# Kernel tuning notes

Measured on AMD Instinct MI355X. Metric: run time of the kernel, lower is better.

The kernel has to match this reference:

```python
import jax, jax.numpy as jnp
import numpy as np

D_MODEL = 1024
NUM_HEADS = 16
DK = D_MODEL // NUM_HEADS
THETA = 10000.0
B, S = 4, 2048


def _rope(x, pos):
    # x: [B, H, S, dk], pos: [S] int positions
    half = DK // 2
    inv_freq = THETA ** (-jnp.arange(half, dtype=jnp.float32) * 2.0 / DK)  # [half]
    ang = pos.astype(jnp.float32)[:, None] * inv_freq[None, :]             # [S, half]
    cos, sin = jnp.cos(ang), jnp.sin(ang)                                  # [S, half]
    x_even = x[..., 0::2]
    x_odd = x[..., 1::2]
    out_even = x_even * cos - x_odd * sin
    out_odd = x_even * sin + x_odd * cos
    # interleave back to [..., dk]
    return jnp.stack([out_even, out_odd], axis=-1).reshape(x.shape)


def setup_inputs() -> dict:
    key = jax.random.key(0)
    ks = jax.random.split(key, 5)
    scale = 1.0 / np.sqrt(D_MODEL)
    return {
        "x": jax.random.normal(ks[0], (B, S, D_MODEL), dtype=jnp.float32),
        "token_position": jnp.arange(S, dtype=jnp.int32),
        "wq": jax.random.normal(ks[1], (D_MODEL, D_MODEL), dtype=jnp.float32) * scale,
        "wk": jax.random.normal(ks[2], (D_MODEL, D_MODEL), dtype=jnp.float32) * scale,
        "wv": jax.random.normal(ks[3], (D_MODEL, D_MODEL), dtype=jnp.float32) * scale,
        "wo": jax.random.normal(ks[4], (D_MODEL, D_MODEL), dtype=jnp.float32) * scale,
    }


def reference(x, token_position, wq, wk, wv, wo):
    b, s, _ = x.shape
    # QKV projections (torch Linear: y = x @ W.T), split heads -> [B, H, S, dk]
    def proj(w):
        y = jnp.einsum("bsd,ed->bse", x, w)
        return y.reshape(b, s, NUM_HEADS, DK).transpose(0, 2, 1, 3)
    q, k, v = proj(wq), proj(wk), proj(wv)
    q = _rope(q, token_position)
    k = _rope(k, token_position)
    # causal SDPA
    scores = jnp.einsum("bhqd,bhkd->bhqk", q, k) / jnp.sqrt(jnp.float32(DK))
    causal = jnp.tril(jnp.ones((s, s), dtype=bool))
    scores = jnp.where(causal, scores, -jnp.inf)
    attn = jax.nn.softmax(scores, axis=-1)
    out = jnp.einsum("bhqk,bhkd->bhqd", attn, v)          # [B, H, S, dv]
    out = out.transpose(0, 2, 1, 3).reshape(b, s, D_MODEL)  # merge heads
    return jnp.einsum("bsd,ed->bse", out, wo)             # output projection
```

## Files before the change

### kernel.cpp

```cpp
#include <hip/hip_runtime.h>


#define D_MODEL 1024
#define NH      16
#define DKH     64
#define SEQ     2048
#define BATCH   4
#define SCALE_LOG2 0.180336875461f
#define ROPE_L2    0.41524101186092029f

typedef _Float16 f16;
typedef _Float16 f16x8 __attribute__((ext_vector_type(8)));
typedef _Float16 f16x4 __attribute__((ext_vector_type(4)));
typedef __fp16   fp16x2n __attribute__((ext_vector_type(2)));
typedef float    f32x4 __attribute__((ext_vector_type(4)));
typedef unsigned short u16;
typedef unsigned int   u32;

__device__ __forceinline__ void glds16(const void* g, void* l) {
  __builtin_amdgcn_global_load_lds((const __attribute__((address_space(1))) void*)g,
                                   (__attribute__((address_space(3))) void*)l, 16, 0, 0);
}
__device__ __forceinline__ u32 pk(float a, float b) {
  union { fp16x2n h; u32 u; } c; c.h = __builtin_amdgcn_cvt_pkrtz(a, b); return c.u;
}

__global__ void cvt_all(const float* __restrict__ x,
                        const float* __restrict__ w0, const float* __restrict__ w1,
                        const float* __restrict__ w2, const float* __restrict__ w3,
                        f16* __restrict__ xo, f16* __restrict__ o0, f16* __restrict__ o1,
                        f16* __restrict__ o2, f16* __restrict__ o3) {
  int blk = blockIdx.x;
  const float* src; f16* dst; int off;
  if (blk < 8192) { src = x; dst = xo; off = blk; }
  else {
    int t = blk - 8192; int w = t >> 10; off = t & 1023;
    switch (w) { case 0: src = w0; dst = o0; break;  case 1: src = w1; dst = o1; break;
                 case 2: src = w2; dst = o2; break;  default: src = w3; dst = o3; break; }
  }
  int i = (off * 256 + threadIdx.x) * 4;
  float4 v = *(const float4*)(src + i);
  uint2 o; o.x = pk(v.x, v.y); o.y = pk(v.z, v.w);
  *(uint2*)(dst + i) = o;
}

#define VMW_(N) asm volatile("s_waitcnt vmcnt(" #N ")" ::: "memory")
#define VMW(N) VMW_(N)

template<int MODE, int CPX, int NBX>
__global__ __launch_bounds__(512, 2) void gemm256(const f16* __restrict__ A,
                                                  const f16* __restrict__ W,
                                                  void* __restrict__ C0,
                                                  void* __restrict__ C1,
                                                  void* __restrict__ C2,
                                                  const int* __restrict__ pos) {
  extern __shared__ char lds[];
  const int bid  = blockIdx.x;
  const int lin  = (bid & 7) * CPX + (bid >> 3);
  const int bx   = lin % NBX, by = lin / NBX;
  const int m0   = by * 256, n0 = bx * 256;
  const int tid  = threadIdx.x;
  const int wave = tid >> 6, lane = tid & 63;
  const int quad = lane >> 4, l16 = lane & 15;
  const int wr   = wave >> 2, wc = wave & 3;

  f32x4 acc[8][4];
#pragma unroll
  for (int i = 0; i < 8; ++i)
#pragma unroll
    for (int j = 0; j < 4; ++j) acc[i][j] = (f32x4){0.f, 0.f, 0.f, 0.f};

  const int posR = (l16 & 1) * 4 + (quad ^ ((l16 >> 1) & 3));
  const char* aRd = lds + wr * 8192 + (l16 >> 1) * 128 + posR * 16;
  const char* bRd = lds + 65536 + wc * 4096 + (l16 >> 1) * 128 + posR * 16;

  const int r0 = 2 * (tid >> 3) + ((tid & 7) >> 2);
  const int c0 = (tid & 3) ^ ((tid >> 3) & 3);
  const f16* pA0 = A + (size_t)(m0 + r0) * 1024 + c0 * 8;
  const f16* pA1 = pA0 + (size_t)128 * 1024;
  const f16* pB0 = W + (size_t)(n0 + r0) * 1024 + c0 * 8;
  const f16* pB1 = pB0 + (size_t)128 * 1024;
  char* const sdA = lds + (size_t)(tid & 448) * 16;
  char* const sdB = lds + 65536 + (size_t)(tid & 448) * 16;

#define ST_A(TB, H) do {                                                      \
    glds16(pA0 + (H) * 32, sdA + (TB) * 32768 + (H) * 16384);                 \
    glds16(pA1 + (H) * 32, sdA + (TB) * 32768 + (H) * 16384 + 8192);          \
  } while (0)
#define ST_B(TB, H) do {                                                      \
    glds16(pB0 + (H) * 32, sdB + (TB) * 32768 + (H) * 16384);                 \
    glds16(pB1 + (H) * 32, sdB + (TB) * 32768 + (H) * 16384 + 8192);          \
  } while (0)
#define RDA(BUF, H, MG) do { _Pragma("unroll")                                \
    for (int i_ = 0; i_ < 4; ++i_)                                            \
      af[i_] = *(const f16x8*)(aRd + (BUF) * 32768 + (H) * 16384 +            \
                               (MG) * 4096 + i_ * 1024);                      \
  } while (0)
#define RDB(BUF, H) do { _Pragma("unroll")                                    \
    for (int j_ = 0; j_ < 4; ++j_)                                            \
      bf[j_] = *(const f16x8*)(bRd + (BUF) * 32768 + (H) * 16384 + j_ * 1024);\
  } while (0)
#define MM(MG) do { _Pragma("unroll")                                         \
    for (int i_ = 0; i_ < 4; ++i_) { _Pragma("unroll")                        \
      for (int j_ = 0; j_ < 4; ++j_)                                          \
        acc[(MG) * 4 + i_][j_] = __builtin_amdgcn_mfma_f32_16x16x32_f16(      \
            af[i_], bf[j_], acc[(MG) * 4 + i_][j_], 0, 0, 0); }               \
  } while (0)
#define PRE_MFMA() do {                                                       \
    __builtin_amdgcn_s_barrier();                                             \
    asm volatile("s_waitcnt lgkmcnt(0)" ::: "memory");                        \
    __builtin_amdgcn_sched_barrier(0);                                        \
  } while (0)

#define TILE(BUF, DOSTAGE, VM2, VM4, LAST) do {                               \
    f16x8 af[4], bf[4];                                                       \
    RDA(BUF, 0, 0); RDB(BUF, 0);                                              \
    if (DOSTAGE) ST_A((BUF) ^ 1, 0);                                          \
    PRE_MFMA();                                                               \
    __builtin_amdgcn_s_setprio(1); MM(0); __builtin_amdgcn_s_setprio(0);      \
    __builtin_amdgcn_s_barrier();                                             \
    RDA(BUF, 0, 1);                                                           \
    if (DOSTAGE) ST_B((BUF) ^ 1, 0);                                          \
    PRE_MFMA();                                                               \
    __builtin_amdgcn_s_setprio(1); MM(1); __builtin_amdgcn_s_setprio(0);      \
    VMW(VM2); __builtin_amdgcn_sched_barrier(0);                              \
    __builtin_amdgcn_s_barrier();                                             \
    RDA(BUF, 1, 0); RDB(BUF, 1);                                              \
    if (DOSTAGE) ST_A((BUF) ^ 1, 1);                                          \
    PRE_MFMA();                                                               \
    __builtin_amdgcn_s_setprio(1); MM(0); __builtin_amdgcn_s_setprio(0);      \
    __builtin_amdgcn_s_barrier();                                             \
    RDA(BUF, 1, 1);                                                           \
    if (DOSTAGE) ST_B((BUF) ^ 1, 1);                                          \
    PRE_MFMA();                                                               \
    __builtin_amdgcn_s_setprio(1); MM(1); __builtin_amdgcn_s_setprio(0);      \
    if (!(LAST)) {                                                            \
      VMW(VM4); __builtin_amdgcn_sched_barrier(0);                            \
      __builtin_amdgcn_s_barrier();                                           \
    }                                                                         \
    if (DOSTAGE) { pA0 += 64; pA1 += 64; pB0 += 64; pB1 += 64; }              \
  } while (0)

  ST_A(0, 0); ST_B(0, 0); ST_A(0, 1); ST_B(0, 1);
  pA0 += 64; pA1 += 64; pB0 += 64; pB1 += 64;
  VMW(4); __builtin_amdgcn_sched_barrier(0);
  __builtin_amdgcn_s_barrier();

#pragma unroll 1
  for (int it = 0; it < 7; ++it) {
    TILE(0, 1, 4, 4, 0);
    TILE(1, 1, 4, 4, 0);
  }
  TILE(0, 1, 4, 4, 0);
  TILE(1, 0, 0, 0, 1);

#undef TILE
#undef PRE_MFMA
#undef MM
#undef RDB
#undef RDA
#undef ST_B
#undef ST_A

  if (MODE == 1) {
    f16* dst; int nb;
    if (bx < 4)      { dst = (f16*)C0; nb = n0; }
    else if (bx < 8) { dst = (f16*)C1; nb = n0 - 1024; }
    else             { dst = (f16*)C2; nb = n0 - 2048; }
    if (bx < 8) {
      float invf[4], sgn[4];
#pragma unroll
      for (int ni = 0; ni < 4; ++ni) {
        int dk = (wc * 64 + ni * 16 + l16) & 63;
        invf[ni] = __builtin_amdgcn_exp2f(-ROPE_L2 * (float)(dk >> 1));
        sgn[ni]  = (dk & 1) ? 1.f : -1.f;
      }
#pragma unroll
      for (int a = 0; a < 8; ++a)
#pragma unroll
        for (int r = 0; r < 4; ++r) {
          int row = m0 + wr * 128 + a * 16 + quad * 4 + r;
          float ps = (float)pos[row & (SEQ - 1)];
#pragma unroll
          for (int ni = 0; ni < 4; ++ni) {
            float ang = ps * invf[ni];
            float c = __cosf(ang), sn = __sinf(ang);
            float v = acc[a][ni][r];
            float p = __shfl_xor(v, 1);
            float ov = fmaf(p * sgn[ni], sn, v * c);
            int col = nb + wc * 64 + ni * 16 + l16;
            dst[(size_t)row * 1024 + col] = (f16)ov;
          }
        }
    } else {
#pragma unroll
      for (int a = 0; a < 8; ++a)
#pragma unroll
        for (int ni = 0; ni < 4; ++ni)
#pragma unroll
          for (int r = 0; r < 4; ++r) {
            int row = m0 + wr * 128 + a * 16 + quad * 4 + r;
            int col = nb + wc * 64 + ni * 16 + l16;
            dst[(size_t)row * 1024 + col] = (f16)acc[a][ni][r];
          }
    }
  } else {
    float* dst = (float*)C0;
#pragma unroll
    for (int a = 0; a < 8; ++a)
#pragma unroll
      for (int ni = 0; ni < 4; ++ni)
#pragma unroll
        for (int r = 0; r < 4; ++r) {
          int row = m0 + wr * 128 + a * 16 + quad * 4 + r;
          int col = n0 + wc * 64 + ni * 16 + l16;
          dst[(size_t)row * 1024 + col] = acc[a][ni][r];
        }
  }
}

__global__ __launch_bounds__(256, 3) void flash_attn(const f16* __restrict__ Q,
                                                     const f16* __restrict__ Kg,
                                                     const f16* __restrict__ Vg,
                                                     f16* __restrict__ O) {
  __shared__ char smem[38400];
  f16*  KsL         = (f16*)smem;
  u32   (*Vt)[67]   = (u32(*)[67])(smem + 16384);
  float (*Red0)[66] = (float(*)[66])smem;
  float (*Red1)[66] = (float(*)[66])(smem + 16896);
  float (*Lb)[17]   = (float(*)[17])(smem + 33792);

  const int tid  = threadIdx.x;
  const int bh   = blockIdx.x;
  const int b    = bh >> 4, h = bh & 15;
  const int qblk = 31 - (int)blockIdx.y;
  const int q0   = qblk * 64;
  const int wave = tid >> 6, lane = tid & 63;
  const int quad = lane >> 4, l16 = lane & 15;
  const int nkt  = (qblk + 2) >> 1;

  f16x8 qf[4][2];
#pragma unroll
  for (int nt = 0; nt < 4; ++nt)
#pragma unroll
    for (int ks = 0; ks < 2; ++ks) {
      f16x8 qv = *(const f16x8*)(Q + ((size_t)(b * SEQ + q0 + nt * 16 + l16)) * D_MODEL
                                   + h * DKH + ks * 32 + quad * 8);
      qf[nt][ks] = qv * (f16)SCALE_LOG2;
    }

  f32x4 o[4][4];
#pragma unroll
  for (int md = 0; md < 4; ++md)
#pragma unroll
    for (int nt = 0; nt < 4; ++nt) o[md][nt] = (f32x4){0.f, 0.f, 0.f, 0.f};
  float lacc[4] = {0.f, 0.f, 0.f, 0.f};

  const int kp = tid >> 3, dc = (tid & 7) * 8;

  for (int t = 0; t < nkt; ++t) {
    const int kt = t * 128;
    const f16* vb = Vg + ((size_t)(b * SEQ + kt + 2 * kp)) * D_MODEL + h * DKH + dc;
    uint4 v0 = *(const uint4*)vb;
    uint4 v1 = *(const uint4*)(vb + D_MODEL);
    uint4 v2 = *(const uint4*)(vb + 64 * D_MODEL);
    uint4 v3 = *(const uint4*)(vb + 65 * D_MODEL);

    if (t) __syncthreads();
#pragma unroll
    for (int i = 0; i < 4; ++i) {
      int ci = i * 256 + tid;
      int row = ci >> 3, gc = (ci & 7) ^ (row & 7);
      glds16(Kg + ((size_t)(b * SEQ + kt + row)) * D_MODEL + h * DKH + gc * 8,
             smem + (size_t)(i * 256 + (tid & 192)) * 16);
    }
    {
      union { uint4 u; u16 s[8]; } a0, a1, a2, a3;
      a0.u = v0; a1.u = v1; a2.u = v2; a3.u = v3;
#pragma unroll
      for (int j = 0; j < 8; ++j) {
        Vt[dc + j][kp]      = (u32)a0.s[j] | ((u32)a1.s[j] << 16);
        Vt[dc + j][32 + kp] = (u32)a2.s[j] | ((u32)a3.s[j] << 16);
      }
    }
    __syncthreads();

    f16x4 pb[2][4];
#pragma unroll
    for (int mt = 0; mt < 2; ++mt) {
      const int krow = wave * 32 + mt * 16 + l16;
      const int s0 = quad ^ (krow & 7);
      f16x8 ka0 = *(const f16x8*)(KsL + krow * 64 + s0 * 8);
      f16x8 ka1 = *(const f16x8*)(KsL + krow * 64 + (s0 ^ 4) * 8);
      const int keyb = kt + wave * 32 + mt * 16 + quad * 4;
#pragma unroll
      for (int nt = 0; nt < 4; ++nt) {
        f32x4 c = (f32x4){0.f, 0.f, 0.f, 0.f};
        c = __builtin_amdgcn_mfma_f32_16x16x32_f16(ka0, qf[nt][0], c, 0, 0, 0);
        c = __builtin_amdgcn_mfma_f32_16x16x32_f16(ka1, qf[nt][1], c, 0, 0, 0);
        const int q = q0 + nt * 16 + l16;
        float p0 = __builtin_amdgcn_exp2f(c[0]);
        float p1 = __builtin_amdgcn_exp2f(c[1]);
        float p2 = __builtin_amdgcn_exp2f(c[2]);
        float p3 = __builtin_amdgcn_exp2f(c[3]);
        if (t == nkt - 1) {
          p0 = (keyb + 0 <= q) ? p0 : 0.f;
          p1 = (keyb + 1 <= q) ? p1 : 0.f;
          p2 = (keyb + 2 <= q) ? p2 : 0.f;
          p3 = (keyb + 3 <= q) ? p3 : 0.f;
        }
        lacc[nt] += (p0 + p1) + (p2 + p3);
        union { u32 w[2]; f16x4 v; } pp;
        pp.w[0] = pk(p0, p1); pp.w[1] = pk(p2, p3);
        pb[mt][nt] = pp.v;
      }
    }

#pragma unroll
    for (int md = 0; md < 4; ++md)
#pragma unroll
      for (int ks2 = 0; ks2 < 2; ++ks2) {
        const u32* vp = &Vt[md * 16 + l16][wave * 16 + ks2 * 8 + quad * 2];
        union { u32 x[2]; f16x4 v; } va;
        va.x[0] = vp[0]; va.x[1] = vp[1];
#pragma unroll
        for (int nt = 0; nt < 4; ++nt)
          o[md][nt] = __builtin_amdgcn_mfma_f32_16x16x16f16(va.v, pb[ks2][nt], o[md][nt], 0, 0, 0);
      }
  }

  __syncthreads();
  {
    float (*Rw)[66] = (wave >= 2) ? Red1 : Red0;
    if ((wave & 1) == 0) {
#pragma unroll
      for (int md = 0; md < 4; ++md)
#pragma unroll
        for (int nt = 0; nt < 4; ++nt)
#pragma unroll
          for (int r = 0; r < 4; ++r)
            Rw[md * 16 + quad * 4 + r][nt * 16 + l16] = o[md][nt][r];
    }
#pragma unroll
    for (int nt = 0; nt < 4; ++nt)
      Lb[nt * 16 + l16][wave * 4 + quad] = lacc[nt];
    __syncthreads();
    if (wave & 1) {
#pragma unroll
      for (int md = 0; md < 4; ++md)
#pragma unroll
        for (int nt = 0; nt < 4; ++nt)
#pragma unroll
          for (int r = 0; r < 4; ++r)
            Rw[md * 16 + quad * 4 + r][nt * 16 + l16] += o[md][nt][r];
    }
    __syncthreads();
  }

  {
    const int q = tid & 63, dc4 = (tid >> 6) * 16;
    float lsum = 0.f;
#pragma unroll
    for (int j = 0; j < 16; ++j) lsum += Lb[q][j];
    float linv = __builtin_amdgcn_rcpf(lsum);
    union { uint4 u[2]; u32 w[8]; } ov;
#pragma unroll
    for (int i = 0; i < 8; ++i) {
      float f0 = Red0[dc4 + 2 * i][q]     + Red1[dc4 + 2 * i][q];
      float f1 = Red0[dc4 + 2 * i + 1][q] + Red1[dc4 + 2 * i + 1][q];
      ov.w[i] = pk(f0 * linv, f1 * linv);
    }
    f16* op = O + ((size_t)(b * SEQ + q0 + q)) * D_MODEL + h * DKH + dc4;
    *(uint4*)op = ov.u[0];
    *(uint4*)(op + 8) = ov.u[1];
  }
}

extern "C" void kernel_launch(void* const* d_in, const int* in_sizes, int n_in,
                              void* d_out, int out_size, void* d_ws, size_t ws_size,
                              hipStream_t stream) {
  const float* x      = (const float*)d_in[0];
  const int*   tokpos = (const int*)d_in[1];
  const float* wq     = (const float*)d_in[2];
  const float* wk     = (const float*)d_in[3];
  const float* wv     = (const float*)d_in[4];
  const float* wo     = (const float*)d_in[5];
  float* out = (float*)d_out;

  char* ws = (char*)d_ws;
  f16* Xb  = (f16*)(ws + 0);
  f16* Wqb = (f16*)(ws + 16777216);
  f16* Wkb = (f16*)(ws + 18874368);
  f16* Wvb = (f16*)(ws + 20971520);
  f16* Wob = (f16*)(ws + 23068672);
  f16* Qb  = (f16*)(ws + 25165824);
  f16* Kb  = (f16*)(ws + 41943040);
  f16* Vb  = (f16*)(ws + 58720256);
  f16* Ob  = Xb;

  static bool attr_done = false;
  if (!attr_done) {
    auto* f1 = gemm256<1, 48, 12>;
    auto* f0 = gemm256<0, 16, 4>;
    (void)hipFuncSetAttribute(reinterpret_cast<const void*>(f1),
                              hipFuncAttributeMaxDynamicSharedMemorySize, 131072);
    (void)hipFuncSetAttribute(reinterpret_cast<const void*>(f0),
                              hipFuncAttributeMaxDynamicSharedMemorySize, 131072);
    attr_done = true;
  }

  cvt_all<<<12288, 256, 0, stream>>>(x, wq, wk, wv, wo, Xb, Wqb, Wkb, Wvb, Wob);

  gemm256<1, 48, 12><<<384, 512, 131072, stream>>>(Xb, Wqb, Qb, Kb, Vb, tokpos);

  flash_attn<<<dim3(BATCH * NH, 32), 256, 0, stream>>>(Qb, Kb, Vb, Ob);

  gemm256<0, 16, 4><<<128, 512, 131072, stream>>>(Ob, Wob, out, nullptr, nullptr, tokpos);
}
```

Before: 259.2 us.

## Retile QKV and output GEMMs to fill all CUs with 256x192 and 128x256 tiles

The QKV projection GEMM moves from 256x256 tiles (384 blocks) to 256x192 tiles (512 blocks). This needs a new B-operand LDS layout with 3 loads per stage and a per-column Q/K/V segment dispatch in the RoPE epilogue. The output projection GEMM moves from 256x256 (128 blocks) to 128x256 tiles (256 blocks) with its own pipeline. The aim is to give the 256 CUs an even wave count and better occupancy, at the cost of less reuse per tile and new swizzle/wait-count logic that could be wrong.

```diff
diff --git a/kernel.cpp b/kernel.cpp
--- a/kernel.cpp
+++ b/kernel.cpp
@@ -24,6 +24,14 @@
 __device__ __forceinline__ u32 pk(float a, float b) {
   union { fp16x2n h; u32 u; } c; c.h = __builtin_amdgcn_cvt_pkrtz(a, b); return c.u;
 }
+
+#define VMW_(N) asm volatile("s_waitcnt vmcnt(" #N ")" ::: "memory")
+#define VMW(N) VMW_(N)
+#define PRE_MFMA() do {                                                       \
+    __builtin_amdgcn_s_barrier();                                             \
+    asm volatile("s_waitcnt lgkmcnt(0)" ::: "memory");                        \
+    __builtin_amdgcn_sched_barrier(0);                                        \
+  } while (0)
 
 __global__ void cvt_all(const float* __restrict__ x,
                         const float* __restrict__ w0, const float* __restrict__ w1,
@@ -44,42 +52,42 @@
   *(uint2*)(dst + i) = o;
 }
 
-#define VMW_(N) asm volatile("s_waitcnt vmcnt(" #N ")" ::: "memory")
-#define VMW(N) VMW_(N)
-
-template<int MODE, int CPX, int NBX>
-__global__ __launch_bounds__(512, 2) void gemm256(const f16* __restrict__ A,
-                                                  const f16* __restrict__ W,
-                                                  void* __restrict__ C0,
-                                                  void* __restrict__ C1,
-                                                  void* __restrict__ C2,
-                                                  const int* __restrict__ pos) {
+__global__ __launch_bounds__(512, 2) void gemm_qkv(const f16* __restrict__ A,
+                                                   const f16* __restrict__ W,
+                                                   f16* __restrict__ Qo,
+                                                   f16* __restrict__ Ko,
+                                                   f16* __restrict__ Vo,
+                                                   const int* __restrict__ pos) {
   extern __shared__ char lds[];
   const int bid  = blockIdx.x;
-  const int lin  = (bid & 7) * CPX + (bid >> 3);
-  const int bx   = lin % NBX, by = lin / NBX;
-  const int m0   = by * 256, n0 = bx * 256;
+  const int lin  = (bid & 7) * 64 + (bid >> 3);
+  const int bx   = lin & 15, by = lin >> 4;
+  const int m0   = by * 256, n0 = bx * 192;
   const int tid  = threadIdx.x;
   const int wave = tid >> 6, lane = tid & 63;
   const int quad = lane >> 4, l16 = lane & 15;
   const int wr   = wave >> 2, wc = wave & 3;
 
-  f32x4 acc[8][4];
+  f32x4 acc[8][3];
 #pragma unroll
   for (int i = 0; i < 8; ++i)
 #pragma unroll
-    for (int j = 0; j < 4; ++j) acc[i][j] = (f32x4){0.f, 0.f, 0.f, 0.f};
+    for (int j = 0; j < 3; ++j) acc[i][j] = (f32x4){0.f, 0.f, 0.f, 0.f};
 
   const int posR = (l16 & 1) * 4 + (quad ^ ((l16 >> 1) & 3));
-  const char* aRd = lds + wr * 8192 + (l16 >> 1) * 128 + posR * 16;
-  const char* bRd = lds + 65536 + wc * 4096 + (l16 >> 1) * 128 + posR * 16;
-
-  const int r0 = 2 * (tid >> 3) + ((tid & 7) >> 2);
-  const int c0 = (tid & 3) ^ ((tid >> 3) & 3);
-  const f16* pA0 = A + (size_t)(m0 + r0) * 1024 + c0 * 8;
+  const char* aRd  = lds + wr * 8192 + (l16 >> 1) * 128 + posR * 16;
+  const char* bRd0 = lds + 65536 + (wc * 48 + l16) * 128 + ((quad) ^ (l16 & 7)) * 16;
+  const char* bRd1 = lds + 65536 + (wc * 48 + l16) * 128 + ((4 + quad) ^ (l16 & 7)) * 16;
+
+  const int srA = tid >> 3;
+  const int rA  = 2 * srA + ((tid >> 2) & 1);
+  const int cA  = (tid & 3) ^ (srA & 3);
+  const f16* pA0 = A + (size_t)(m0 + rA) * 1024 + cA * 8;
   const f16* pA1 = pA0 + (size_t)128 * 1024;
-  const f16* pB0 = W + (size_t)(n0 + r0) * 1024 + c0 * 8;
-  const f16* pB1 = pB0 + (size_t)128 * 1024;
+  const int gB = (tid & 7) ^ ((tid >> 3) & 7);
+  const f16* pB0 = W + (size_t)(n0 + (tid >> 3)) * 1024 + gB * 8;
+  const f16* pB1 = pB0 + (size_t)64 * 1024;
+  const f16* pB2 = pB0 + (size_t)128 * 1024;
   char* const sdA = lds + (size_t)(tid & 448) * 16;
   char* const sdB = lds + 65536 + (size_t)(tid & 448) * 16;
 
@@ -87,9 +95,10 @@
     glds16(pA0 + (H) * 32, sdA + (TB) * 32768 + (H) * 16384);                 \
     glds16(pA1 + (H) * 32, sdA + (TB) * 32768 + (H) * 16384 + 8192);          \
   } while (0)
-#define ST_B(TB, H) do {                                                      \
-    glds16(pB0 + (H) * 32, sdB + (TB) * 32768 + (H) * 16384);                 \
-    glds16(pB1 + (H) * 32, sdB + (TB) * 32768 + (H) * 16384 + 8192);          \
+#define ST_B(TB) do {                                                         \
+    glds16(pB0, sdB + (TB) * 24576);                                          \
+    glds16(pB1, sdB + (TB) * 24576 + 8192);                                   \
+    glds16(pB2, sdB + (TB) * 24576 + 16384);                                  \
   } while (0)
 #define RDA(BUF, H, MG) do { _Pragma("unroll")                                \
     for (int i_ = 0; i_ < 4; ++i_)                                            \
@@ -97,126 +106,187 @@
                                (MG) * 4096 + i_ * 1024);                      \
   } while (0)
 #define RDB(BUF, H) do { _Pragma("unroll")                                    \
-    for (int j_ = 0; j_ < 4; ++j_)                                            \
-      bf[j_] = *(const f16x8*)(bRd + (BUF) * 32768 + (H) * 16384 + j_ * 1024);\
-  } while (0)
-#define MM(MG) do { _Pragma("unroll")                                         \
+    for (int j_ = 0; j_ < 3; ++j_)                                            \
+      bf[j_] = *(const f16x8*)(((H) ? bRd1 : bRd0) + (BUF) * 24576 + j_ * 2048);\
+  } while (0)
+#define MMQ(MG) do {                                                          \
+    __builtin_amdgcn_s_setprio(1);                                            \
+    _Pragma("unroll")                                                         \
     for (int i_ = 0; i_ < 4; ++i_) { _Pragma("unroll")                        \
-      for (int j_ = 0; j_ < 4; ++j_)                                          \
+      for (int j_ = 0; j_ < 3; ++j_)                                          \
         acc[(MG) * 4 + i_][j_] = __builtin_amdgcn_mfma_f32_16x16x32_f16(      \
             af[i_], bf[j_], acc[(MG) * 4 + i_][j_], 0, 0, 0); }               \
-  } while (0)
-#define PRE_MFMA() do {                                                       \
-    __builtin_amdgcn_s_barrier();                                             \
-    asm volatile("s_waitcnt lgkmcnt(0)" ::: "memory");                        \
-    __builtin_amdgcn_sched_barrier(0);                                        \
-  } while (0)
-
-#define TILE(BUF, DOSTAGE, VM2, VM4, LAST) do {                               \
-    f16x8 af[4], bf[4];                                                       \
+    __builtin_amdgcn_s_setprio(0);                                            \
+  } while (0)
+
+#define TILE(BUF, DOSTAGE, VM2, LAST) do {                                    \
+    f16x8 af[4]; f16x8 bf[3];                                                 \
     RDA(BUF, 0, 0); RDB(BUF, 0);                                              \
     if (DOSTAGE) ST_A((BUF) ^ 1, 0);                                          \
-    PRE_MFMA();                                                               \
-    __builtin_amdgcn_s_setprio(1); MM(0); __builtin_amdgcn_s_setprio(0);      \
+    PRE_MFMA(); MMQ(0);                                                       \
     __builtin_amdgcn_s_barrier();                                             \
     RDA(BUF, 0, 1);                                                           \
-    if (DOSTAGE) ST_B((BUF) ^ 1, 0);                                          \
-    PRE_MFMA();                                                               \
-    __builtin_amdgcn_s_setprio(1); MM(1); __builtin_amdgcn_s_setprio(0);      \
+    if (DOSTAGE) ST_B((BUF) ^ 1);                                             \
+    PRE_MFMA(); MMQ(1);                                                       \
     VMW(VM2); __builtin_amdgcn_sched_barrier(0);                              \
     __builtin_amdgcn_s_barrier();                                             \
     RDA(BUF, 1, 0); RDB(BUF, 1);                                              \
     if (DOSTAGE) ST_A((BUF) ^ 1, 1);                                          \
-    PRE_MFMA();                                                               \
-    __builtin_amdgcn_s_setprio(1); MM(0); __builtin_amdgcn_s_setprio(0);      \
+    PRE_MFMA(); MMQ(0);                                                       \
     __builtin_amdgcn_s_barrier();                                             \
     RDA(BUF, 1, 1);                                                           \
-    if (DOSTAGE) ST_B((BUF) ^ 1, 1);                                          \
-    PRE_MFMA();                                                               \
-    __builtin_amdgcn_s_setprio(1); MM(1); __builtin_amdgcn_s_setprio(0);      \
+    PRE_MFMA(); MMQ(1);                                                       \
     if (!(LAST)) {                                                            \
-      VMW(VM4); __builtin_amdgcn_sched_barrier(0);                            \
+      VMW_(2); __builtin_amdgcn_sched_barrier(0);                             \
       __builtin_amdgcn_s_barrier();                                           \
     }                                                                         \
-    if (DOSTAGE) { pA0 += 64; pA1 += 64; pB0 += 64; pB1 += 64; }              \
-  } while (0)
-
-  ST_A(0, 0); ST_B(0, 0); ST_A(0, 1); ST_B(0, 1);
-  pA0 += 64; pA1 += 64; pB0 += 64; pB1 += 64;
-  VMW(4); __builtin_amdgcn_sched_barrier(0);
+    if (DOSTAGE) { pA0 += 64; pA1 += 64; pB0 += 64; pB1 += 64; pB2 += 64; }   \
+  } while (0)
+
+  ST_A(0, 0); ST_B(0); ST_A(0, 1);
+  pA0 += 64; pA1 += 64; pB0 += 64; pB1 += 64; pB2 += 64;
+  VMW_(2); __builtin_amdgcn_sched_barrier(0);
   __builtin_amdgcn_s_barrier();
 
 #pragma unroll 1
   for (int it = 0; it < 7; ++it) {
-    TILE(0, 1, 4, 4, 0);
-    TILE(1, 1, 4, 4, 0);
-  }
-  TILE(0, 1, 4, 4, 0);
-  TILE(1, 0, 0, 0, 1);
+    TILE(0, 1, 5, 0);
+    TILE(1, 1, 5, 0);
+  }
+  TILE(0, 1, 5, 0);
+  TILE(1, 0, 0, 1);
 
 #undef TILE
-#undef PRE_MFMA
-#undef MM
+#undef MMQ
 #undef RDB
 #undef RDA
 #undef ST_B
 #undef ST_A
 
-  if (MODE == 1) {
-    f16* dst; int nb;
-    if (bx < 4)      { dst = (f16*)C0; nb = n0; }
-    else if (bx < 8) { dst = (f16*)C1; nb = n0 - 1024; }
-    else             { dst = (f16*)C2; nb = n0 - 2048; }
-    if (bx < 8) {
-      float invf[4], sgn[4];
-#pragma unroll
-      for (int ni = 0; ni < 4; ++ni) {
-        int dk = (wc * 64 + ni * 16 + l16) & 63;
-        invf[ni] = __builtin_amdgcn_exp2f(-ROPE_L2 * (float)(dk >> 1));
-        sgn[ni]  = (dk & 1) ? 1.f : -1.f;
+  f16* dsts[3]; int colB[3]; bool rp[3]; float invf[3], sgn[3];
+#pragma unroll
+  for (int ni = 0; ni < 3; ++ni) {
+    int gc  = n0 + wc * 48 + ni * 16 + l16;
+    int seg = gc >> 10;
+    dsts[ni] = (seg == 0) ? Qo : (seg == 1) ? Ko : Vo;
+    colB[ni] = gc & 1023;
+    rp[ni]   = (seg < 2);
+    int dk   = gc & 63;
+    invf[ni] = __builtin_amdgcn_exp2f(-ROPE_L2 * (float)(dk >> 1));
+    sgn[ni]  = (dk & 1) ? 1.f : -1.f;
+  }
+#pragma unroll
+  for (int a = 0; a < 8; ++a)
+#pragma unroll
+    for (int r = 0; r < 4; ++r) {
+      int row = m0 + wr * 128 + a * 16 + quad * 4 + r;
+      float ps = (float)pos[row & (SEQ - 1)];
+#pragma unroll
+      for (int ni = 0; ni < 3; ++ni) {
+        float v = acc[a][ni][r];
+        float ov;
+        if (rp[ni]) {
+          float ang = ps * invf[ni];
+          float c = __cosf(ang), sn = __sinf(ang);
+          float p = __shfl_xor(v, 1);
+          ov = fmaf(p * sgn[ni], sn, v * c);
+        } else ov = v;
+        dsts[ni][(size_t)row * 1024 + colB[ni]] = (f16)ov;
       }
-#pragma unroll
-      for (int a = 0; a < 8; ++a)
-#pragma unroll
-        for (int r = 0; r < 4; ++r) {
-          int row = m0 + wr * 128 + a * 16 + quad * 4 + r;
-          float ps = (float)pos[row & (SEQ - 1)];
-#pragma unroll
-          for (int ni = 0; ni < 4; ++ni) {
-            float ang = ps * invf[ni];
-            float c = __cosf(ang), sn = __sinf(ang);
-            float v = acc[a][ni][r];
-            float p = __shfl_xor(v, 1);
-            float ov = fmaf(p * sgn[ni], sn, v * c);
-            int col = nb + wc * 64 + ni * 16 + l16;
-            dst[(size_t)row * 1024 + col] = (f16)ov;
-          }
-        }
-    } else {
-#pragma unroll
-      for (int a = 0; a < 8; ++a)
-#pragma unroll
-        for (int ni = 0; ni < 4; ++ni)
-#pragma unroll
-          for (int r = 0; r < 4; ++r) {
-            int row = m0 + wr * 128 + a * 16 + quad * 4 + r;
-            int col = nb + wc * 64 + ni * 16 + l16;
-            dst[(size_t)row * 1024 + col] = (f16)acc[a][ni][r];
-          }
-    }
-  } else {
-    float* dst = (float*)C0;
-#pragma unroll
-    for (int a = 0; a < 8; ++a)
-#pragma unroll
-      for (int ni = 0; ni < 4; ++ni)
-#pragma unroll
-        for (int r = 0; r < 4; ++r) {
-          int row = m0 + wr * 128 + a * 16 + quad * 4 + r;
-          int col = n0 + wc * 64 + ni * 16 + l16;
-          dst[(size_t)row * 1024 + col] = acc[a][ni][r];
-        }
-  }
+    }
+}
+
+__global__ __launch_bounds__(512, 2) void gemm_out(const f16* __restrict__ A,
+                                                   const f16* __restrict__ W,
+                                                   float* __restrict__ C) {
+  extern __shared__ char lds[];
+  const int bid  = blockIdx.x;
+  const int lin  = (bid & 7) * 32 + (bid >> 3);
+  const int bx   = lin & 3, by = lin >> 2;
+  const int m0   = by * 128, n0 = bx * 256;
+  const int tid  = threadIdx.x;
+  const int wave = tid >> 6, lane = tid & 63;
+  const int quad = lane >> 4, l16 = lane & 15;
+  const int wr   = wave >> 2, wc = wave & 3;
+
+  f32x4 acc[4][4];
+#pragma unroll
+  for (int i = 0; i < 4; ++i)
+#pragma unroll
+    for (int j = 0; j < 4; ++j) acc[i][j] = (f32x4){0.f, 0.f, 0.f, 0.f};
+
+  const int posR = (l16 & 1) * 4 + (quad ^ ((l16 >> 1) & 3));
+  const char* aRd = lds + wr * 4096 + (l16 >> 1) * 128 + posR * 16;
+  const char* bRd = lds + 32768 + wc * 4096 + (l16 >> 1) * 128 + posR * 16;
+
+  const int srA = tid >> 3;
+  const int rA  = 2 * srA + ((tid >> 2) & 1);
+  const int cA  = (tid & 3) ^ (srA & 3);
+  const f16* pA = A + (size_t)(m0 + rA) * 1024 + cA * 8;
+  const int rB  = 2 * (tid >> 3) + ((tid >> 2) & 1);
+  const int cB  = (tid & 3) ^ ((tid >> 3) & 3);
+  const f16* pB0 = W + (size_t)(n0 + rB) * 1024 + cB * 8;
+  const f16* pB1 = pB0 + (size_t)128 * 1024;
+  char* const sdA = lds + (size_t)(tid & 448) * 16;
+  char* const sdB = lds + 32768 + (size_t)(tid & 448) * 16;
+
+#define ST_AO(TB, H) glds16(pA + (H) * 32, sdA + (TB) * 16384 + (H) * 8192)
+#define ST_BO(TB, H) do {                                                     \
+    glds16(pB0 + (H) * 32, sdB + (TB) * 32768 + (H) * 16384);                 \
+    glds16(pB1 + (H) * 32, sdB + (TB) * 32768 + (H) * 16384 + 8192);          \
+  } while (0)
+#define HALF(BUF, H, DOSTAGE, VMN, LAST) do {                                 \
+    f16x8 af[4], bf[4];                                                       \
+    _Pragma("unroll")                                                         \
+    for (int i_ = 0; i_ < 4; ++i_)                                            \
+      af[i_] = *(const f16x8*)(aRd + (BUF) * 16384 + (H) * 8192 + i_ * 1024); \
+    _Pragma("unroll")                                                         \
+    for (int j_ = 0; j_ < 4; ++j_)                                            \
+      bf[j_] = *(const f16x8*)(bRd + (BUF) * 32768 + (H) * 16384 + j_ * 1024);\
+    if (DOSTAGE) { ST_AO((BUF) ^ 1, H); ST_BO((BUF) ^ 1, H); }                \
+    PRE_MFMA();                                                               \
+    __builtin_amdgcn_s_setprio(1);                                            \
+    _Pragma("unroll")                                                         \
+    for (int i_ = 0; i_ < 4; ++i_) { _Pragma("unroll")                        \
+      for (int j_ = 0; j_ < 4; ++j_)                                          \
+        acc[i_][j_] = __builtin_amdgcn_mfma_f32_16x16x32_f16(                 \
+            af[i_], bf[j_], acc[i_][j_], 0, 0, 0); }                          \
+    __builtin_amdgcn_s_setprio(0);                                            \
+    if (!(LAST)) {                                                            \
+      VMW(VMN); __builtin_amdgcn_sched_barrier(0);                            \
+      __builtin_amdgcn_s_barrier();                                           \
+    }                                                                         \
+  } while (0)
+
+  ST_AO(0, 0); ST_BO(0, 0); ST_AO(0, 1); ST_BO(0, 1);
+  pA += 64; pB0 += 64; pB1 += 64;
+  VMW_(3); __builtin_amdgcn_sched_barrier(0);
+  __builtin_amdgcn_s_barrier();
+
+#pragma unroll 1
+  for (int it = 0; it < 7; ++it) {
+    HALF(0, 0, 1, 3, 0); HALF(0, 1, 1, 3, 0); pA += 64; pB0 += 64; pB1 += 64;
+    HALF(1, 0, 1, 3, 0); HALF(1, 1, 1, 3, 0); pA += 64; pB0 += 64; pB1 += 64;
+  }
+  HALF(0, 0, 1, 3, 0); HALF(0, 1, 1, 3, 0);
+  HALF(1, 0, 0, 0, 0);
+  HALF(1, 1, 0, 0, 1);
+
+#undef HALF
+#undef ST_BO
+#undef ST_AO
+
+  float* dst = C;
+#pragma unroll
+  for (int a = 0; a < 4; ++a)
+#pragma unroll
+    for (int ni = 0; ni < 4; ++ni)
+#pragma unroll
+      for (int r = 0; r < 4; ++r) {
+        int row = m0 + wr * 64 + a * 16 + quad * 4 + r;
+        int col = n0 + wc * 64 + ni * 16 + l16;
+        dst[(size_t)row * 1024 + col] = acc[a][ni][r];
+      }
 }
 
 __global__ __launch_bounds__(256, 3) void flash_attn(const f16* __restrict__ Q,
@@ -400,20 +470,18 @@
 
   static bool attr_done = false;
   if (!attr_done) {
-    auto* f1 = gemm256<1, 48, 12>;
-    auto* f0 = gemm256<0, 16, 4>;
-    (void)hipFuncSetAttribute(reinterpret_cast<const void*>(f1),
-                              hipFuncAttributeMaxDynamicSharedMemorySize, 131072);
-    (void)hipFuncSetAttribute(reinterpret_cast<const void*>(f0),
-                              hipFuncAttributeMaxDynamicSharedMemorySize, 131072);
+    (void)hipFuncSetAttribute(reinterpret_cast<const void*>(gemm_qkv),
+                              hipFuncAttributeMaxDynamicSharedMemorySize, 114688);
+    (void)hipFuncSetAttribute(reinterpret_cast<const void*>(gemm_out),
+                              hipFuncAttributeMaxDynamicSharedMemorySize, 98304);
     attr_done = true;
   }
 
   cvt_all<<<12288, 256, 0, stream>>>(x, wq, wk, wv, wo, Xb, Wqb, Wkb, Wvb, Wob);
 
-  gemm256<1, 48, 12><<<384, 512, 131072, stream>>>(Xb, Wqb, Qb, Kb, Vb, tokpos);
+  gemm_qkv<<<512, 512, 114688, stream>>>(Xb, Wqb, Qb, Kb, Vb, tokpos);
 
   flash_attn<<<dim3(BATCH * NH, 32), 256, 0, stream>>>(Qb, Kb, Vb, Ob);
 
-  gemm256<0, 16, 4><<<128, 512, 131072, stream>>>(Ob, Wob, out, nullptr, nullptr, tokpos);
-}
+  gemm_out<<<256, 512, 98304, stream>>>(Ob, Wob, out);
+}
```

New measurement: 246.6 us. 1.05x faster.
